# Kernel tuning notes

Hardware: AMD Instinct MI355X
Metric: run time of the kernel (lower is better)

Reference implementation:

```python
import jax, jax.numpy as jnp
import numpy as np

B, L, D, H, NB = 4, 1024, 512, 8, 128
HD = D // H
EPS = 1e-6


def rmsnorm(x, w):
    v = jnp.mean(x * x, axis=-1, keepdims=True)
    return x * jax.lax.rsqrt(v + EPS) * w


def setup_inputs() -> dict:
    key = jax.random.key(0)
    ks = jax.random.split(key, 9)
    hidden_states = jax.random.normal(ks[0], (B, L, D), dtype=jnp.float32)
    # sorted unix-like timestamps (int32 to avoid x64 requirement)
    timestamps = jnp.sort(jax.random.randint(ks[1], (B, L), 0, 1_000_000, dtype=jnp.int32), axis=1)
    # causal mask (True = attend)
    attention_mask = jnp.broadcast_to(jnp.tril(jnp.ones((L, L), dtype=bool)), (B, 1, L, L))
    w = lambda k, sh: jax.random.normal(k, sh, dtype=jnp.float32) * 0.02
    return {
        'hidden_states': hidden_states,
        'attention_mask': attention_mask,
        'timestamps': timestamps,
        'ln_w': jnp.ones((D,), jnp.float32),
        'attn_ln_w': jnp.ones((D,), jnp.float32),
        'wq': w(ks[2], (D, D)),
        'wk': w(ks[3], (D, D)),
        'wv': w(ks[4], (D, D)),
        'wu': w(ks[5], (D, D)),
        'wo': w(ks[6], (D, D)),
        'ts_w': w(ks[7], (NB + 1,)),
        'pos_w': w(ks[8], (2 * L - 1,)),
    }


def rel_attn_bias(timestamps, ts_w, pos_w):
    # relative position bias: bias_pos[i, j] = pos_w[(L-1) + j - i]
    i = jnp.arange(L)
    idx = (L - 1) + i[None, :] - i[:, None]  # [L, L]
    pos_bias = pos_w[idx]  # [L, L]
    # bucketized relative time bias (HSTU): diff[b,i,j] = ext[b,i+1] - ext[b,j]
    ext = jnp.concatenate([timestamps, timestamps[:, -1:]], axis=1)  # [B, L+1]
    diff = ext[:, 1:, None] - ext[:, None, :-1]  # [B, L, L]
    logd = jnp.log(jnp.clip(jnp.abs(diff).astype(jnp.float32), 1.0, None)) / 0.301
    bucket = jnp.clip(logd.astype(jnp.int32), 0, NB)  # floor via int cast (logd >= 0)
    ts_bias = ts_w[bucket]  # [B, L, L]
    return ts_bias + pos_bias[None]  # [B, L, L]


def reference(hidden_states, attention_mask, timestamps, ln_w, attn_ln_w, wq, wk, wv, wu, wo, ts_w, pos_w):
    residual = hidden_states
    h = rmsnorm(hidden_states, ln_w)  # [B, L, D]
    q = jax.nn.silu(h @ wq.T).reshape(B, L, H, HD)
    k = jax.nn.silu(h @ wk.T).reshape(B, L, H, HD)
    v = jax.nn.silu(h @ wv.T).reshape(B, L, H, HD)
    qk = jnp.einsum('bihd,bjhd->bhij', q, k)  # [B, H, L, L]
    qk = qk + rel_attn_bias(timestamps, ts_w, pos_w)[:, None]  # broadcast over heads
    attn = jax.nn.silu(qk) / L
    attn = attn * attention_mask.astype(attn.dtype)
    attn_out = jnp.einsum('bhij,bjhd->bihd', attn, v).reshape(B, L, D)
    u = jax.nn.silu(h @ wu.T)
    gated = u * rmsnorm(attn_out, attn_ln_w)
    out = residual + gated @ wo.T
    return out, attn
```

## Files before the change

kernel.cpp:

```cpp
#include <hip/hip_runtime.h>
#include <hip/hip_bf16.h>

typedef __hip_bfloat16 bf16;
typedef __attribute__((ext_vector_type(8))) short short8;
typedef __attribute__((ext_vector_type(4))) float f32x4;

#define SL 1024
#define DIM 512
#define NH 8
#define HD 64
#define NBUCK 128

__device__ __forceinline__ float silu_f(float x) { return x / (1.0f + __expf(-x)); }

__device__ __forceinline__ short f2bf(float x) {
  bf16 b = __float2bfloat16(x);
  return *reinterpret_cast<short*>(&b);
}

__device__ __forceinline__ void gld_lds16(const void* g, void* l) {
  __builtin_amdgcn_global_load_lds(
      (const __attribute__((address_space(1))) void*)g,
      (__attribute__((address_space(3))) void*)l, 16, 0, 0);
}

__global__ __launch_bounds__(256) void prep_k(const float* __restrict__ s0, const float* __restrict__ s1,
                                              const float* __restrict__ s2, const float* __restrict__ s3,
                                              const float* __restrict__ s4, bf16* __restrict__ wdst,
                                              const float* __restrict__ hidden, const float* __restrict__ ln_w,
                                              bf16* __restrict__ hb) {
  int bx = blockIdx.x;
  if (bx < 1280) {
    int wsel = bx >> 8;
    const float* src = wsel == 0 ? s0 : wsel == 1 ? s1 : wsel == 2 ? s2 : wsel == 3 ? s3 : s4;
    int i = ((bx & 255) * 256 + threadIdx.x) * 4;
    float4 v = *(const float4*)(src + i);
    bf16* d = wdst + (size_t)wsel * DIM * DIM + i;
    d[0] = __float2bfloat16(v.x);
    d[1] = __float2bfloat16(v.y);
    d[2] = __float2bfloat16(v.z);
    d[3] = __float2bfloat16(v.w);
  } else {
    int row = (bx - 1280) * 4 + (threadIdx.x >> 6);
    int l = threadIdx.x & 63;
    const float4* xr = (const float4*)(hidden + (size_t)row * DIM);
    float4 v0 = xr[l], v1 = xr[l + 64];
    float s = v0.x*v0.x + v0.y*v0.y + v0.z*v0.z + v0.w*v0.w
            + v1.x*v1.x + v1.y*v1.y + v1.z*v1.z + v1.w*v1.w;
    #pragma unroll
    for (int o = 32; o; o >>= 1) s += __shfl_xor(s, o);
    float sc = rsqrtf(s * (1.0f / DIM) + 1e-6f);
    bf16* orow = hb + (size_t)row * DIM;
    int c0 = l * 4, c1 = 256 + l * 4;
    orow[c0 + 0] = __float2bfloat16(v0.x * sc * ln_w[c0 + 0]);
    orow[c0 + 1] = __float2bfloat16(v0.y * sc * ln_w[c0 + 1]);
    orow[c0 + 2] = __float2bfloat16(v0.z * sc * ln_w[c0 + 2]);
    orow[c0 + 3] = __float2bfloat16(v0.w * sc * ln_w[c0 + 3]);
    orow[c1 + 0] = __float2bfloat16(v1.x * sc * ln_w[c1 + 0]);
    orow[c1 + 1] = __float2bfloat16(v1.y * sc * ln_w[c1 + 1]);
    orow[c1 + 2] = __float2bfloat16(v1.z * sc * ln_w[c1 + 2]);
    orow[c1 + 3] = __float2bfloat16(v1.w * sc * ln_w[c1 + 3]);
  }
}

__device__ __forceinline__ void gemm128_core64(const bf16* __restrict__ A,
                                               const bf16* __restrict__ Bt,
                                               short* lds, int bm, int bn,
                                               f32x4 acc[4][4]) {
  int t = threadIdx.x, w = t >> 6, l = t & 63;
  int ln = l & 15;
  int wr = (w >> 1) * 64, wc = (w & 1) * 64;
  int srow8 = l >> 3;
  int scol = ((l & 7) ^ srow8) * 8;
  for (int kt = 0; kt < 8; ++kt) {
    if (kt) __syncthreads();
    #pragma unroll
    for (int i = 0; i < 8; ++i) {
      int s = i * 4 + w;
      int row = (s & 15) * 8 + srow8;
      int col = kt * 64 + scol;
      const bf16* gsrc = (s < 16)
          ? (A  + (size_t)(bm * 128 + row) * DIM + col)
          : (Bt + (size_t)(bn * 128 + row) * DIM + col);
      gld_lds16(gsrc, lds + s * 512 + l * 8);
    }
    __syncthreads();
    #pragma unroll
    for (int kk = 0; kk < 2; ++kk) {
      short8 a[4], b[4];
      #pragma unroll
      for (int m = 0; m < 4; ++m) {
        int row = wr + m * 16 + ln;
        int c = ((kk * 4 + (l >> 4)) ^ (row & 7)) * 8;
        a[m] = *(const short8*)(lds + row * 64 + c);
      }
      #pragma unroll
      for (int n = 0; n < 4; ++n) {
        int row = wc + n * 16 + ln;
        int c = ((kk * 4 + (l >> 4)) ^ (row & 7)) * 8;
        b[n] = *(const short8*)(lds + 8192 + row * 64 + c);
      }
      #pragma unroll
      for (int m = 0; m < 4; ++m)
        #pragma unroll
        for (int n = 0; n < 4; ++n)
          acc[m][n] = __builtin_amdgcn_mfma_f32_16x16x32_bf16(a[m], b[n], acc[m][n], 0, 0, 0);
    }
  }
}

__global__ __launch_bounds__(256) void gemm_qkvu_k(const bf16* __restrict__ hb,
                                                   const bf16* __restrict__ wb,
                                                   bf16* __restrict__ q, bf16* __restrict__ k,
                                                   bf16* __restrict__ vT, bf16* __restrict__ u) {
  __shared__ __align__(16) short lds[16384];
  int mode = blockIdx.y;
  int bm = blockIdx.x & 31, bn = blockIdx.x >> 5;
  f32x4 acc[4][4];
  #pragma unroll
  for (int m = 0; m < 4; ++m)
    #pragma unroll
    for (int n = 0; n < 4; ++n) { f32x4 z = {0.f, 0.f, 0.f, 0.f}; acc[m][n] = z; }
  gemm128_core64(hb, wb + (size_t)mode * DIM * DIM, lds, bm, bn, acc);

  int t = threadIdx.x, w = t >> 6, l = t & 63;
  int ln = l & 15, l4 = (l >> 4) * 4;
  int wr = (w >> 1) * 64, wc = (w & 1) * 64;

  if (mode == 2) {
    int b = bm >> 3, li0 = (bm & 7) * 128;
    #pragma unroll
    for (int hc = 0; hc < 2; ++hc) {
      __syncthreads();
      if ((w & 1) == hc) {
        #pragma unroll
        for (int m = 0; m < 4; ++m)
          #pragma unroll
          for (int n = 0; n < 4; ++n)
            #pragma unroll
            for (int j = 0; j < 4; ++j) {
              int rl = wr + m * 16 + l4 + j;
              int cl = n * 16 + ln;
              lds[rl * 65 + cl] = f2bf(silu_f(acc[m][n][j]));
            }
      }
      __syncthreads();
      int hh = bn * 2 + hc;
      int d = t >> 2, seg = t & 3;
      bf16* dst = vT + ((size_t)(b * NH + hh) * HD + d) * SL + li0 + seg * 32;
      short8 y0, y1, y2, y3;
      #pragma unroll
      for (int qq = 0; qq < 8; ++qq) {
        y0[qq] = lds[(seg * 32 + qq) * 65 + d];
        y1[qq] = lds[(seg * 32 + 8 + qq) * 65 + d];
        y2[qq] = lds[(seg * 32 + 16 + qq) * 65 + d];
        y3[qq] = lds[(seg * 32 + 24 + qq) * 65 + d];
      }
      *(short8*)dst = y0; *(short8*)(dst + 8) = y1;
      *(short8*)(dst + 16) = y2; *(short8*)(dst + 24) = y3;
    }
    return;
  }

  #pragma unroll
  for (int m = 0; m < 4; ++m)
    #pragma unroll
    for (int n = 0; n < 4; ++n)
      #pragma unroll
      for (int j = 0; j < 4; ++j) {
        int rg = bm * 128 + wr + m * 16 + l4 + j;
        int cg = bn * 128 + wc + n * 16 + ln;
        bf16 val = __float2bfloat16(silu_f(acc[m][n][j]));
        int b = rg >> 10, li = rg & 1023, hh = cg >> 6, dd = cg & 63;
        if (mode == 0)      q[((size_t)(b * NH + hh) * SL + li) * HD + dd] = val;
        else if (mode == 1) k[((size_t)(b * NH + hh) * SL + li) * HD + dd] = val;
        else                u[(size_t)rg * DIM + cg] = val;
      }
}

__global__ __launch_bounds__(256) void qk_attn_k(const bf16* __restrict__ q,
                                                 const bf16* __restrict__ k,
                                                 const int* __restrict__ ts,
                                                 const float* __restrict__ ts_w,
                                                 const float* __restrict__ pos_w,
                                                 float* __restrict__ attn) {
  int bh = blockIdx.y, x = blockIdx.x;
  int ti = 0, accx = 0;
  while (accx + ti + 1 <= x) { accx += ti + 1; ++ti; }
  int tj = x - accx;
  int t = threadIdx.x, w = t >> 6, l = t & 63;
  int ln = l & 15, l4 = (l >> 4) * 4;
  int wr = (w >> 1) * 64, wc = (w & 1) * 64;
  float* arow = attn + (size_t)bh * SL * SL;

  __shared__ __align__(16) short lds[16384];
  __shared__ float tw_l[NBUCK + 1];
  __shared__ float pw_l[255];
  __shared__ int tsi_l[128], tsj_l[128];

  const int* tsb = ts + (size_t)(bh >> 3) * SL;
  if (t < NBUCK + 1) tw_l[t] = ts_w[t];
  if (t < 255) pw_l[t] = pos_w[896 + (tj - ti) * 128 + t];
  if (t < 128) tsi_l[t] = tsb[min(ti * 128 + t + 1, SL - 1)];
  else         tsj_l[t - 128] = tsb[tj * 128 + (t - 128)];

  #pragma unroll
  for (int i = 0; i < 8; ++i) {
    int s = i * 4 + w;
    int row = (s & 15) * 8 + (l >> 3);
    int col = ((l & 7) ^ (l >> 3)) * 8;
    const bf16* g = (s < 16)
        ? (q + (size_t)bh * SL * HD + (size_t)(ti * 128 + row) * HD + col)
        : (k + (size_t)bh * SL * HD + (size_t)(tj * 128 + row) * HD + col);
    gld_lds16(g, lds + s * 512 + l * 8);
  }
  __syncthreads();

  f32x4 acc[4][4];
  #pragma unroll
  for (int m = 0; m < 4; ++m)
    #pragma unroll
    for (int n = 0; n < 4; ++n) { f32x4 z = {0.f, 0.f, 0.f, 0.f}; acc[m][n] = z; }
  #pragma unroll
  for (int kk = 0; kk < 2; ++kk) {
    short8 a[4], b[4];
    #pragma unroll
    for (int m = 0; m < 4; ++m) {
      int row = wr + m * 16 + ln;
      int c = ((kk * 4 + (l >> 4)) ^ (row & 7)) * 8;
      a[m] = *(const short8*)(lds + row * 64 + c);
    }
    #pragma unroll
    for (int n = 0; n < 4; ++n) {
      int row = wc + n * 16 + ln;
      int c = ((kk * 4 + (l >> 4)) ^ (row & 7)) * 8;
      b[n] = *(const short8*)(lds + 8192 + row * 64 + c);
    }
    #pragma unroll
    for (int m = 0; m < 4; ++m)
      #pragma unroll
      for (int n = 0; n < 4; ++n)
        acc[m][n] = __builtin_amdgcn_mfma_f32_16x16x32_bf16(a[m], b[n], acc[m][n], 0, 0, 0);
  }

  const float LSC = 2.30281455f;
  #pragma unroll
  for (int m = 0; m < 4; ++m)
    #pragma unroll
    for (int j = 0; j < 4; ++j) {
      int il = wr + m * 16 + l4 + j;
      int tsi = tsi_l[il];
      int i = ti * 128 + il;
      #pragma unroll
      for (int n = 0; n < 4; ++n) {
        int jl = wc + n * 16 + ln;
        int jj = tj * 128 + jl;
        float v = acc[m][n][j];
        int dt = tsi - tsj_l[jl];
        float adf = fmaxf(fabsf((float)dt), 1.0f);
        int bucket = (int)(__log2f(adf) * LSC);
        bucket = bucket < 0 ? 0 : (bucket > NBUCK ? NBUCK : bucket);
        float bias = tw_l[bucket] + pw_l[jl - il + 127];
        float o = (jj <= i) ? silu_f(v + bias) * (1.0f / (float)SL) : 0.0f;
        arow[(size_t)i * SL + jj] = o;
      }
    }

  if (x < 28) {
    int zi = 0, acc2 = 0;
    while (acc2 + (7 - zi) <= x) { acc2 += 7 - zi; ++zi; }
    int zj = zi + 1 + (x - acc2);
    float4 z4 = make_float4(0.f, 0.f, 0.f, 0.f);
    #pragma unroll
    for (int rep = 0; rep < 16; ++rep) {
      int flat = rep * 256 + t;
      int row = flat >> 5, c4 = flat & 31;
      *(float4*)(arow + (size_t)(zi * 128 + row) * SL + zj * 128 + c4 * 4) = z4;
    }
  }
}

__global__ __launch_bounds__(256) void pv_k(const float* __restrict__ attn,
                                            const bf16* __restrict__ vT,
                                            float* __restrict__ ao0,
                                            float* __restrict__ ao1) {
  int bh = blockIdx.y, bm = blockIdx.x, sp = blockIdx.z;
  int t = threadIdx.x, w = t >> 6, l = t & 63;
  int ln = l & 15, l4 = (l >> 4) * 4;
  __shared__ __align__(16) short lds[12288];
  const float* arow = attn + (size_t)bh * SL * SL;
  const bf16* vrow = vT + (size_t)bh * HD * SL;
  f32x4 acc[2][4];
  #pragma unroll
  for (int m = 0; m < 2; ++m)
    #pragma unroll
    for (int n = 0; n < 4; ++n) { f32x4 z = {0.f, 0.f, 0.f, 0.f}; acc[m][n] = z; }

  int srow8 = l >> 3;
  int swc = ((l & 7) ^ srow8) * 8;
  int klo = sp * (bm + 1);
  int khi = klo + (bm + 1);
  for (int kt = klo; kt < khi; ++kt) {
    if (kt > klo) __syncthreads();
    #pragma unroll
    for (int ss = 0; ss < 4; ++ss) {
      int s = w * 4 + ss;
      int row = s * 8 + srow8;
      const float* g = arow + (size_t)(bm * 128 + row) * SL + kt * 64 + (l & 7) * 8;
      float4 f0 = *(const float4*)g;
      float4 f1 = *(const float4*)(g + 4);
      short8 vv;
      vv[0] = f2bf(f0.x); vv[1] = f2bf(f0.y); vv[2] = f2bf(f0.z); vv[3] = f2bf(f0.w);
      vv[4] = f2bf(f1.x); vv[5] = f2bf(f1.y); vv[6] = f2bf(f1.z); vv[7] = f2bf(f1.w);
      *(short8*)(lds + row * 64 + swc) = vv;
    }
    #pragma unroll
    for (int i = 0; i < 2; ++i) {
      int s2 = i * 4 + w;
      int row = s2 * 8 + srow8;
      gld_lds16(vrow + (size_t)row * SL + kt * 64 + swc, lds + 8192 + s2 * 512 + l * 8);
    }
    __syncthreads();
    #pragma unroll
    for (int kk = 0; kk < 2; ++kk) {
      short8 a[2], b[4];
      #pragma unroll
      for (int m = 0; m < 2; ++m) {
        int row = w * 32 + m * 16 + ln;
        int c = ((kk * 4 + (l >> 4)) ^ (row & 7)) * 8;
        a[m] = *(const short8*)(lds + row * 64 + c);
      }
      #pragma unroll
      for (int n = 0; n < 4; ++n) {
        int row = n * 16 + ln;
        int c = ((kk * 4 + (l >> 4)) ^ (row & 7)) * 8;
        b[n] = *(const short8*)(lds + 8192 + row * 64 + c);
      }
      #pragma unroll
      for (int m = 0; m < 2; ++m)
        #pragma unroll
        for (int n = 0; n < 4; ++n)
          acc[m][n] = __builtin_amdgcn_mfma_f32_16x16x32_bf16(a[m], b[n], acc[m][n], 0, 0, 0);
    }
  }

  float* aop = sp == 0 ? ao0 : ao1;
  int b = bh >> 3, hh = bh & 7;
  #pragma unroll
  for (int m = 0; m < 2; ++m)
    #pragma unroll
    for (int n = 0; n < 4; ++n)
      #pragma unroll
      for (int j = 0; j < 4; ++j) {
        int i = bm * 128 + w * 32 + m * 16 + l4 + j;
        int dd = n * 16 + ln;
        aop[((size_t)(b * SL + i)) * DIM + hh * HD + dd] = acc[m][n][j];
      }
}

__global__ void gated_k(const float* __restrict__ ao0, const float* __restrict__ ao1,
                        const bf16* __restrict__ u,
                        const float* __restrict__ w, bf16* __restrict__ g) {
  int row = blockIdx.x, l = threadIdx.x;
  const float4* ar0 = (const float4*)(ao0 + (size_t)row * DIM);
  const float4* ar1 = (const float4*)(ao1 + (size_t)row * DIM);
  float4 p0 = ar0[l], p1 = ar1[l], p2 = ar0[l + 64], p3 = ar1[l + 64];
  float4 a0 = make_float4(p0.x + p1.x, p0.y + p1.y, p0.z + p1.z, p0.w + p1.w);
  float4 a1 = make_float4(p2.x + p3.x, p2.y + p3.y, p2.z + p3.z, p2.w + p3.w);
  float s = a0.x*a0.x + a0.y*a0.y + a0.z*a0.z + a0.w*a0.w
          + a1.x*a1.x + a1.y*a1.y + a1.z*a1.z + a1.w*a1.w;
  #pragma unroll
  for (int o = 32; o; o >>= 1) s += __shfl_xor(s, o);
  float sc = rsqrtf(s * (1.0f / DIM) + 1e-6f);
  const bf16* ur = u + (size_t)row * DIM;
  bf16* gr = g + (size_t)row * DIM;
  int c0 = l * 4, c1 = 256 + l * 4;
  gr[c0 + 0] = __float2bfloat16(__bfloat162float(ur[c0 + 0]) * a0.x * sc * w[c0 + 0]);
  gr[c0 + 1] = __float2bfloat16(__bfloat162float(ur[c0 + 1]) * a0.y * sc * w[c0 + 1]);
  gr[c0 + 2] = __float2bfloat16(__bfloat162float(ur[c0 + 2]) * a0.z * sc * w[c0 + 2]);
  gr[c0 + 3] = __float2bfloat16(__bfloat162float(ur[c0 + 3]) * a0.w * sc * w[c0 + 3]);
  gr[c1 + 0] = __float2bfloat16(__bfloat162float(ur[c1 + 0]) * a1.x * sc * w[c1 + 0]);
  gr[c1 + 1] = __float2bfloat16(__bfloat162float(ur[c1 + 1]) * a1.y * sc * w[c1 + 1]);
  gr[c1 + 2] = __float2bfloat16(__bfloat162float(ur[c1 + 2]) * a1.z * sc * w[c1 + 2]);
  gr[c1 + 3] = __float2bfloat16(__bfloat162float(ur[c1 + 3]) * a1.w * sc * w[c1 + 3]);
}

__global__ __launch_bounds__(256) void gemm_out_k(const bf16* __restrict__ gated,
                                                  const bf16* __restrict__ wob,
                                                  const float* __restrict__ residual,
                                                  float* __restrict__ out) {
  int bm = blockIdx.x & 31, bn = blockIdx.x >> 5;
  int t = threadIdx.x, w = t >> 6, l = t & 63;
  int ln = l & 15, l4 = (l >> 4) * 4;
  __shared__ __align__(16) short lds[12288];
  f32x4 acc[2][4];
  #pragma unroll
  for (int m = 0; m < 2; ++m)
    #pragma unroll
    for (int n = 0; n < 4; ++n) { f32x4 z = {0.f, 0.f, 0.f, 0.f}; acc[m][n] = z; }

  int srow8 = l >> 3;
  int scol = ((l & 7) ^ srow8) * 8;
  for (int kt = 0; kt < 8; ++kt) {
    if (kt) __syncthreads();
    #pragma unroll
    for (int i = 0; i < 6; ++i) {
      int s = i * 4 + w;
      int row = (s < 16 ? s : s - 16) * 8 + srow8;
      int col = kt * 64 + scol;
      const bf16* g = (s < 16)
          ? (gated + (size_t)(bm * 128 + row) * DIM + col)
          : (wob + (size_t)(bn * 64 + row) * DIM + col);
      gld_lds16(g, lds + s * 512 + l * 8);
    }
    __syncthreads();
    #pragma unroll
    for (int kk = 0; kk < 2; ++kk) {
      short8 a[2], b[4];
      #pragma unroll
      for (int m = 0; m < 2; ++m) {
        int row = w * 32 + m * 16 + ln;
        int c = ((kk * 4 + (l >> 4)) ^ (row & 7)) * 8;
        a[m] = *(const short8*)(lds + row * 64 + c);
      }
      #pragma unroll
      for (int n = 0; n < 4; ++n) {
        int row = n * 16 + ln;
        int c = ((kk * 4 + (l >> 4)) ^ (row & 7)) * 8;
        b[n] = *(const short8*)(lds + 8192 + row * 64 + c);
      }
      #pragma unroll
      for (int m = 0; m < 2; ++m)
        #pragma unroll
        for (int n = 0; n < 4; ++n)
          acc[m][n] = __builtin_amdgcn_mfma_f32_16x16x32_bf16(a[m], b[n], acc[m][n], 0, 0, 0);
    }
  }

  #pragma unroll
  for (int m = 0; m < 2; ++m)
    #pragma unroll
    for (int n = 0; n < 4; ++n)
      #pragma unroll
      for (int j = 0; j < 4; ++j) {
        int rg = bm * 128 + w * 32 + m * 16 + l4 + j;
        int cg = bn * 64 + n * 16 + ln;
        size_t idx = (size_t)rg * DIM + cg;
        out[idx] = acc[m][n][j] + residual[idx];
      }
}

extern "C" void kernel_launch(void* const* d_in, const int* in_sizes, int n_in,
                              void* d_out, int out_size, void* d_ws, size_t ws_size,
                              hipStream_t stream) {
  const float* hidden    = (const float*)d_in[0];
  const int*   ts        = (const int*)d_in[2];
  const float* ln_w      = (const float*)d_in[3];
  const float* attn_ln_w = (const float*)d_in[4];
  const float* wq        = (const float*)d_in[5];
  const float* wk        = (const float*)d_in[6];
  const float* wv        = (const float*)d_in[7];
  const float* wu        = (const float*)d_in[8];
  const float* wo        = (const float*)d_in[9];
  const float* ts_w      = (const float*)d_in[10];
  const float* pos_w     = (const float*)d_in[11];

  float* out  = (float*)d_out;
  float* attn = out + 2097152;

  bf16* wb    = (bf16*)d_ws;
  bf16* hb    = wb + 5 * DIM * DIM;
  bf16* q     = hb + 2097152;
  bf16* k     = q + 2097152;
  bf16* vT    = k + 2097152;
  bf16* u     = vT + 2097152;
  bf16* gated = u + 2097152;
  float* ao0  = (float*)(gated + 2097152);
  float* ao1  = ao0 + 2097152;

  prep_k<<<2304, 256, 0, stream>>>(wq, wk, wv, wu, wo, wb, hidden, ln_w, hb);
  gemm_qkvu_k<<<dim3(128, 4), 256, 0, stream>>>(hb, wb, q, k, vT, u);
  qk_attn_k<<<dim3(36, 32), 256, 0, stream>>>(q, k, ts, ts_w, pos_w, attn);
  pv_k<<<dim3(8, 32, 2), 256, 0, stream>>>(attn, vT, ao0, ao1);
  gated_k<<<4096, 64, 0, stream>>>(ao0, ao1, u, attn_ln_w, gated);
  gemm_out_k<<<256, 256, 0, stream>>>(gated, wb + 4 * DIM * DIM, hidden, out);
}
```

Baseline: 113.3 us.

## Shrink QKVU GEMM tiles and rebalance causal PV split-K chunks

The QKVU projection GEMM moves from 128x128 to 128x64 output tiles, doubling the grid to 1024 blocks for better CU occupancy. Each tile now covers exactly one head, which simplifies the V-transpose epilogue. The PV kernel replaces its fixed two-way split-K with a 17-chunk schedule that splits the causal lower-triangular work into roughly equal pieces across up to three partial buffers. The third buffer reuses the normalized-hidden workspace, and gated_k sums only the partials that exist for each row block. This trades extra partial-buffer traffic and some GEMM tile reuse for better load balance.

```diff
diff --git a/kernel.cpp b/kernel.cpp
--- a/kernel.cpp
+++ b/kernel.cpp
@@ -63,118 +63,102 @@
   }
 }
 
-__device__ __forceinline__ void gemm128_core64(const bf16* __restrict__ A,
-                                               const bf16* __restrict__ Bt,
-                                               short* lds, int bm, int bn,
-                                               f32x4 acc[4][4]) {
+__global__ __launch_bounds__(256) void gemm_qkvu_k(const bf16* __restrict__ hb,
+                                                   const bf16* __restrict__ wb,
+                                                   bf16* __restrict__ q, bf16* __restrict__ k,
+                                                   bf16* __restrict__ vT, bf16* __restrict__ u) {
+  int mode = blockIdx.y;
+  int bm = blockIdx.x & 31, bn = blockIdx.x >> 5;
   int t = threadIdx.x, w = t >> 6, l = t & 63;
-  int ln = l & 15;
-  int wr = (w >> 1) * 64, wc = (w & 1) * 64;
+  int ln = l & 15, l4 = (l >> 4) * 4;
+  __shared__ __align__(16) short lds[12288];
+  const bf16* wbm = wb + (size_t)mode * DIM * DIM;
+  f32x4 acc[2][4];
+  #pragma unroll
+  for (int m = 0; m < 2; ++m)
+    #pragma unroll
+    for (int n = 0; n < 4; ++n) { f32x4 z = {0.f, 0.f, 0.f, 0.f}; acc[m][n] = z; }
+
   int srow8 = l >> 3;
   int scol = ((l & 7) ^ srow8) * 8;
   for (int kt = 0; kt < 8; ++kt) {
     if (kt) __syncthreads();
     #pragma unroll
-    for (int i = 0; i < 8; ++i) {
+    for (int i = 0; i < 6; ++i) {
       int s = i * 4 + w;
-      int row = (s & 15) * 8 + srow8;
+      int row = (s < 16 ? s : s - 16) * 8 + srow8;
       int col = kt * 64 + scol;
-      const bf16* gsrc = (s < 16)
-          ? (A  + (size_t)(bm * 128 + row) * DIM + col)
-          : (Bt + (size_t)(bn * 128 + row) * DIM + col);
-      gld_lds16(gsrc, lds + s * 512 + l * 8);
+      const bf16* g = (s < 16)
+          ? (hb + (size_t)(bm * 128 + row) * DIM + col)
+          : (wbm + (size_t)(bn * 64 + row) * DIM + col);
+      gld_lds16(g, lds + s * 512 + l * 8);
     }
     __syncthreads();
     #pragma unroll
     for (int kk = 0; kk < 2; ++kk) {
-      short8 a[4], b[4];
-      #pragma unroll
-      for (int m = 0; m < 4; ++m) {
-        int row = wr + m * 16 + ln;
+      short8 a[2], b[4];
+      #pragma unroll
+      for (int m = 0; m < 2; ++m) {
+        int row = w * 32 + m * 16 + ln;
         int c = ((kk * 4 + (l >> 4)) ^ (row & 7)) * 8;
         a[m] = *(const short8*)(lds + row * 64 + c);
       }
       #pragma unroll
       for (int n = 0; n < 4; ++n) {
-        int row = wc + n * 16 + ln;
+        int row = n * 16 + ln;
         int c = ((kk * 4 + (l >> 4)) ^ (row & 7)) * 8;
         b[n] = *(const short8*)(lds + 8192 + row * 64 + c);
       }
       #pragma unroll
-      for (int m = 0; m < 4; ++m)
+      for (int m = 0; m < 2; ++m)
         #pragma unroll
         for (int n = 0; n < 4; ++n)
           acc[m][n] = __builtin_amdgcn_mfma_f32_16x16x32_bf16(a[m], b[n], acc[m][n], 0, 0, 0);
     }
   }
-}
-
-__global__ __launch_bounds__(256) void gemm_qkvu_k(const bf16* __restrict__ hb,
-                                                   const bf16* __restrict__ wb,
-                                                   bf16* __restrict__ q, bf16* __restrict__ k,
-                                                   bf16* __restrict__ vT, bf16* __restrict__ u) {
-  __shared__ __align__(16) short lds[16384];
-  int mode = blockIdx.y;
-  int bm = blockIdx.x & 31, bn = blockIdx.x >> 5;
-  f32x4 acc[4][4];
-  #pragma unroll
-  for (int m = 0; m < 4; ++m)
-    #pragma unroll
-    for (int n = 0; n < 4; ++n) { f32x4 z = {0.f, 0.f, 0.f, 0.f}; acc[m][n] = z; }
-  gemm128_core64(hb, wb + (size_t)mode * DIM * DIM, lds, bm, bn, acc);
-
-  int t = threadIdx.x, w = t >> 6, l = t & 63;
-  int ln = l & 15, l4 = (l >> 4) * 4;
-  int wr = (w >> 1) * 64, wc = (w & 1) * 64;
 
   if (mode == 2) {
+    __syncthreads();
+    #pragma unroll
+    for (int m = 0; m < 2; ++m)
+      #pragma unroll
+      for (int n = 0; n < 4; ++n)
+        #pragma unroll
+        for (int j = 0; j < 4; ++j) {
+          int rl = w * 32 + m * 16 + l4 + j;
+          int cl = n * 16 + ln;
+          lds[rl * 65 + cl] = f2bf(silu_f(acc[m][n][j]));
+        }
+    __syncthreads();
     int b = bm >> 3, li0 = (bm & 7) * 128;
-    #pragma unroll
-    for (int hc = 0; hc < 2; ++hc) {
-      __syncthreads();
-      if ((w & 1) == hc) {
-        #pragma unroll
-        for (int m = 0; m < 4; ++m)
-          #pragma unroll
-          for (int n = 0; n < 4; ++n)
-            #pragma unroll
-            for (int j = 0; j < 4; ++j) {
-              int rl = wr + m * 16 + l4 + j;
-              int cl = n * 16 + ln;
-              lds[rl * 65 + cl] = f2bf(silu_f(acc[m][n][j]));
-            }
-      }
-      __syncthreads();
-      int hh = bn * 2 + hc;
-      int d = t >> 2, seg = t & 3;
-      bf16* dst = vT + ((size_t)(b * NH + hh) * HD + d) * SL + li0 + seg * 32;
-      short8 y0, y1, y2, y3;
-      #pragma unroll
-      for (int qq = 0; qq < 8; ++qq) {
-        y0[qq] = lds[(seg * 32 + qq) * 65 + d];
-        y1[qq] = lds[(seg * 32 + 8 + qq) * 65 + d];
-        y2[qq] = lds[(seg * 32 + 16 + qq) * 65 + d];
-        y3[qq] = lds[(seg * 32 + 24 + qq) * 65 + d];
-      }
-      *(short8*)dst = y0; *(short8*)(dst + 8) = y1;
-      *(short8*)(dst + 16) = y2; *(short8*)(dst + 24) = y3;
-    }
+    int d = t >> 2, seg = t & 3;
+    bf16* dst = vT + ((size_t)(b * NH + bn) * HD + d) * SL + li0 + seg * 32;
+    short8 y0, y1, y2, y3;
+    #pragma unroll
+    for (int qq = 0; qq < 8; ++qq) {
+      y0[qq] = lds[(seg * 32 + qq) * 65 + d];
+      y1[qq] = lds[(seg * 32 + 8 + qq) * 65 + d];
+      y2[qq] = lds[(seg * 32 + 16 + qq) * 65 + d];
+      y3[qq] = lds[(seg * 32 + 24 + qq) * 65 + d];
+    }
+    *(short8*)dst = y0; *(short8*)(dst + 8) = y1;
+    *(short8*)(dst + 16) = y2; *(short8*)(dst + 24) = y3;
     return;
   }
 
   #pragma unroll
-  for (int m = 0; m < 4; ++m)
+  for (int m = 0; m < 2; ++m)
     #pragma unroll
     for (int n = 0; n < 4; ++n)
       #pragma unroll
       for (int j = 0; j < 4; ++j) {
-        int rg = bm * 128 + wr + m * 16 + l4 + j;
-        int cg = bn * 128 + wc + n * 16 + ln;
+        int rg = bm * 128 + w * 32 + m * 16 + l4 + j;
+        int c64 = n * 16 + ln;
         bf16 val = __float2bfloat16(silu_f(acc[m][n][j]));
-        int b = rg >> 10, li = rg & 1023, hh = cg >> 6, dd = cg & 63;
-        if (mode == 0)      q[((size_t)(b * NH + hh) * SL + li) * HD + dd] = val;
-        else if (mode == 1) k[((size_t)(b * NH + hh) * SL + li) * HD + dd] = val;
-        else                u[(size_t)rg * DIM + cg] = val;
+        int b = rg >> 10, li = rg & 1023;
+        if (mode == 0)      q[((size_t)(b * NH + bn) * SL + li) * HD + c64] = val;
+        else if (mode == 1) k[((size_t)(b * NH + bn) * SL + li) * HD + c64] = val;
+        else                u[(size_t)rg * DIM + bn * 64 + c64] = val;
       }
 }
 
@@ -283,8 +267,14 @@
 __global__ __launch_bounds__(256) void pv_k(const float* __restrict__ attn,
                                             const bf16* __restrict__ vT,
                                             float* __restrict__ ao0,
-                                            float* __restrict__ ao1) {
-  int bh = blockIdx.y, bm = blockIdx.x, sp = blockIdx.z;
+                                            float* __restrict__ ao1,
+                                            float* __restrict__ ao2) {
+  static const char cb_bm[17] = {0,1,2,2,3,3,4,4,5,5,5,6,6,6,7,7,7};
+  static const char cb_lo[17] = {0,0,0,3,0,4,0,5,0,4,8,0,5,10,0,6,11};
+  static const char cb_hi[17] = {2,4,3,6,4,8,5,10,4,8,12,5,10,14,6,11,16};
+  static const char cb_sl[17] = {0,0,0,1,0,1,0,1,0,1,2,0,1,2,0,1,2};
+  int ch = blockIdx.x, bh = blockIdx.y;
+  int bm = cb_bm[ch], klo = cb_lo[ch], khi = cb_hi[ch], slot = cb_sl[ch];
   int t = threadIdx.x, w = t >> 6, l = t & 63;
   int ln = l & 15, l4 = (l >> 4) * 4;
   __shared__ __align__(16) short lds[12288];
@@ -298,8 +288,6 @@
 
   int srow8 = l >> 3;
   int swc = ((l & 7) ^ srow8) * 8;
-  int klo = sp * (bm + 1);
-  int khi = klo + (bm + 1);
   for (int kt = klo; kt < khi; ++kt) {
     if (kt > klo) __syncthreads();
     #pragma unroll
@@ -344,7 +332,7 @@
     }
   }
 
-  float* aop = sp == 0 ? ao0 : ao1;
+  float* aop = slot == 0 ? ao0 : (slot == 1 ? ao1 : ao2);
   int b = bh >> 3, hh = bh & 7;
   #pragma unroll
   for (int m = 0; m < 2; ++m)
@@ -359,14 +347,24 @@
 }
 
 __global__ void gated_k(const float* __restrict__ ao0, const float* __restrict__ ao1,
-                        const bf16* __restrict__ u,
+                        const float* __restrict__ ao2, const bf16* __restrict__ u,
                         const float* __restrict__ w, bf16* __restrict__ g) {
   int row = blockIdx.x, l = threadIdx.x;
+  int bmRow = (row & 1023) >> 7;
   const float4* ar0 = (const float4*)(ao0 + (size_t)row * DIM);
   const float4* ar1 = (const float4*)(ao1 + (size_t)row * DIM);
-  float4 p0 = ar0[l], p1 = ar1[l], p2 = ar0[l + 64], p3 = ar1[l + 64];
-  float4 a0 = make_float4(p0.x + p1.x, p0.y + p1.y, p0.z + p1.z, p0.w + p1.w);
-  float4 a1 = make_float4(p2.x + p3.x, p2.y + p3.y, p2.z + p3.z, p2.w + p3.w);
+  const float4* ar2 = (const float4*)(ao2 + (size_t)row * DIM);
+  float4 a0 = ar0[l], a1 = ar0[l + 64];
+  if (bmRow >= 2) {
+    float4 p0 = ar1[l], p1 = ar1[l + 64];
+    a0.x += p0.x; a0.y += p0.y; a0.z += p0.z; a0.w += p0.w;
+    a1.x += p1.x; a1.y += p1.y; a1.z += p1.z; a1.w += p1.w;
+  }
+  if (bmRow >= 5) {
+    float4 p0 = ar2[l], p1 = ar2[l + 64];
+    a0.x += p0.x; a0.y += p0.y; a0.z += p0.z; a0.w += p0.w;
+    a1.x += p1.x; a1.y += p1.y; a1.z += p1.z; a1.w += p1.w;
+  }
   float s = a0.x*a0.x + a0.y*a0.y + a0.z*a0.z + a0.w*a0.w
           + a1.x*a1.x + a1.y*a1.y + a1.z*a1.z + a1.w*a1.w;
   #pragma unroll
@@ -477,11 +475,12 @@
   bf16* gated = u + 2097152;
   float* ao0  = (float*)(gated + 2097152);
   float* ao1  = ao0 + 2097152;
+  float* ao2  = (float*)hb;
 
   prep_k<<<2304, 256, 0, stream>>>(wq, wk, wv, wu, wo, wb, hidden, ln_w, hb);
-  gemm_qkvu_k<<<dim3(128, 4), 256, 0, stream>>>(hb, wb, q, k, vT, u);
+  gemm_qkvu_k<<<dim3(256, 4), 256, 0, stream>>>(hb, wb, q, k, vT, u);
   qk_attn_k<<<dim3(36, 32), 256, 0, stream>>>(q, k, ts, ts_w, pos_w, attn);
-  pv_k<<<dim3(8, 32, 2), 256, 0, stream>>>(attn, vT, ao0, ao1);
-  gated_k<<<4096, 64, 0, stream>>>(ao0, ao1, u, attn_ln_w, gated);
+  pv_k<<<dim3(17, 32), 256, 0, stream>>>(attn, vT, ao0, ao1, ao2);
+  gated_k<<<4096, 64, 0, stream>>>(ao0, ao1, ao2, u, attn_ln_w, gated);
   gemm_out_k<<<256, 256, 0, stream>>>(gated, wb + 4 * DIM * DIM, hidden, out);
 }
```

After: 103.7 us, median of 2. 8.5% less time.
